# Optimization experiments

Hardware: AMD Instinct MI355X
Metric: run time of the kernel (lower is better)

Reference implementation:

```python
import jax, jax.numpy as jnp
import numpy as np

C = 128  # hidden_dim


def setup_inputs() -> dict:
    key = jax.random.key(0)
    ks = jax.random.split(key, 8)
    B, H, W = 4, 64, 64
    x1 = jax.random.normal(ks[0], (B, C, H, W), dtype=jnp.float32)
    x2 = jax.random.normal(ks[1], (B, C, H, W), dtype=jnp.float32)
    # 1x1 conv == per-pixel linear over channels; store weights as [C_out, C_in]
    s = 1.0 / np.sqrt(C)
    wq = jax.random.uniform(ks[2], (C, C), jnp.float32, -s, s)
    bq = jax.random.uniform(ks[3], (C,), jnp.float32, -s, s)
    wk = jax.random.uniform(ks[4], (C, C), jnp.float32, -s, s)
    bk = jax.random.uniform(ks[5], (C,), jnp.float32, -s, s)
    wv = jax.random.uniform(ks[6], (C, C), jnp.float32, -s, s)
    bv = jax.random.uniform(ks[7], (C,), jnp.float32, -s, s)
    return {"x1": x1, "x2": x2, "wq": wq, "bq": bq, "wk": wk, "bk": bk, "wv": wv, "bv": bv}


def reference(x1, x2, wq, bq, wk, bk, wv, bv):
    B, Cc, H, W = x1.shape
    N = H * W
    # flatten spatial -> tokens: [B, N, C]
    t1 = x1.reshape(B, Cc, N).transpose(0, 2, 1)
    t2 = x2.reshape(B, Cc, N).transpose(0, 2, 1)
    # 1x1 conv projections (per-token linear)
    q = jnp.einsum('bnc,oc->bno', t1, wq) + bq
    k = jnp.einsum('bnc,oc->bno', t2, wk) + bk
    v = jnp.einsum('bnc,oc->bno', t2, wv) + bv
    scale = 1.0 / jnp.sqrt(jnp.asarray(Cc, x1.dtype))
    attn = jax.nn.softmax(jnp.einsum('bqc,bkc->bqk', q, k) * scale, axis=-1)
    out = jnp.einsum('bqk,bkc->bqc', attn, v)  # [B, N, C]
    out = out.transpose(0, 2, 1).reshape(B, Cc, H, W)
    return out + x1
```

## Files before the change

### kernel.cpp

```cpp
#include <hip/hip_runtime.h>
#include <hip/hip_bf16.h>

typedef float  f32x4  __attribute__((ext_vector_type(4)));
typedef float  f32x16 __attribute__((ext_vector_type(16)));
typedef short  s16x8  __attribute__((ext_vector_type(8)));
typedef int    i32x8  __attribute__((ext_vector_type(8)));
typedef unsigned int   u32x2 __attribute__((ext_vector_type(2)));
typedef unsigned int   u32x4 __attribute__((ext_vector_type(4)));

#define B_ 4
#define C_ 128
#define N_ 4096
#define NST 16
#define QSCALE 0.12751744f

__device__ __forceinline__ unsigned int pkbf(float lo, float hi) {
    union { float f; unsigned int u; } a, b; a.f = lo; b.f = hi;
    return __builtin_amdgcn_perm(b.u + 0x8000u, a.u + 0x8000u, 0x07060302u);
}
__device__ __forceinline__ unsigned int pk_fp8x4(float a, float b, float c, float d) {
    int v = __builtin_amdgcn_cvt_pk_fp8_f32(a, b, 0, false);
    v = __builtin_amdgcn_cvt_pk_fp8_f32(c, d, v, true);
    return (unsigned int)v;
}
__device__ __forceinline__ unsigned int enc_fp4(float v) {
    float m = __builtin_fabsf(v);
    unsigned int c = 0;
    c += m > 0.25f; c += m > 0.75f; c += m > 1.25f; c += m > 1.75f;
    c += m > 2.5f;  c += m > 3.5f;  c += m > 5.0f;
    return c | ((__float_as_uint(v) >> 28) & 8u);
}
__device__ __forceinline__ unsigned int fp4x4(float a, float b, float c, float d) {
    return enc_fp4(a) | (enc_fp4(b) << 4) | (enc_fp4(c) << 8) | (enc_fp4(d) << 12);
}
__device__ __forceinline__ s16x8 mk_frag(unsigned int a, unsigned int b,
                                         unsigned int c, unsigned int d) {
    union { u32x4 u; s16x8 v; } t; t.u = (u32x4){a, b, c, d}; return t.v;
}
__device__ __forceinline__ f32x16 z16() {
    f32x16 v;
    #pragma unroll
    for (int r = 0; r < 16; r++) v[r] = 0.f;
    return v;
}
__device__ __forceinline__ i32x8 ld32g(const unsigned char* p) {
    union { u32x4 q[2]; i32x8 v; } t;
    t.q[0] = *(const u32x4*)p;
    t.q[1] = *(const u32x4*)(p + 1024);
    return t.v;
}
__device__ __forceinline__ i32x8 ld16g(const unsigned char* p) {
    union { u32x4 q[2]; i32x8 v; } t;
    t.q[0] = *(const u32x4*)p;
    t.q[1] = (u32x4){0u, 0u, 0u, 0u};
    return t.v;
}
__device__ __forceinline__ f32x16 mfs4(i32x8 a, i32x8 b, f32x16 c) {
    return __builtin_amdgcn_mfma_scale_f32_32x32x64_f8f6f4(
        a, b, c, 4, 0, 0, 0x7F7F7F7Fu, 0, 0x7F7F7F7Fu);
}

__global__ __launch_bounds__(256) void wcvt_kernel(
    const float* __restrict__ wq, const float* __restrict__ wk,
    const float* __restrict__ wv, unsigned short* __restrict__ Wf)
{
    const int gid = blockIdx.x * 256 + threadIdx.x;
    const int l = gid & 63, fid = gid >> 6;
    const int kc = fid & 7, ot = (fid >> 3) & 3, z = fid >> 5;
    const float* w = (z == 0) ? wq : (z == 1 ? wk : wv);
    const int o  = 32 * ot + (l & 31);
    const int c0 = 16 * kc + 8 * (l >> 5);
    const float* src = &w[o * C_ + c0];
    *(u32x4*)&Wf[fid * 512 + l * 8] = (u32x4){
        pkbf(src[0], src[1]), pkbf(src[2], src[3]),
        pkbf(src[4], src[5]), pkbf(src[6], src[7])};
}

__global__ __launch_bounds__(256, 2) void proj_kernel(
    const float* __restrict__ x1, const float* __restrict__ x2,
    const float* __restrict__ bq, const float* __restrict__ bk,
    const float* __restrict__ bv,
    const unsigned short* __restrict__ Wf,
    unsigned char* __restrict__ Qf, unsigned char* __restrict__ Kf,
    unsigned char* __restrict__ Vf)
{
    __shared__ float Xs[2][C_ * 36];
    const int tid = threadIdx.x;
    const int ot  = tid >> 6;
    const int l = tid & 63, lo = l & 31, h = l >> 5;
    const int bid = blockIdx.x;
    const int b = bid & 3, tb = bid >> 2;
    const int n0 = tb * 32;

    {
        const int q = tid & 7, c0 = tid >> 3;
        #pragma unroll
        for (int cc = 0; cc < 4; cc++) {
            const int c = c0 + 32 * cc;
            const size_t gof = ((size_t)b * C_ + c) * N_ + n0 + 4 * q;
            *(f32x4*)&Xs[0][c * 36 + 4 * q] = *(const f32x4*)&x1[gof];
            *(f32x4*)&Xs[1][c * 36 + 4 * q] = *(const f32x4*)&x2[gof];
        }
    }
    __syncthreads();

    auto ldW = [&](int z, int kc) -> s16x8 {
        return *(const s16x8*)&Wf[(((z * 4 + ot) * 8) + kc) * 512 + l * 8];
    };
    auto xfrag = [&](int z, int kc) -> s16x8 {
        const float* p = &Xs[z][(16 * kc + 8 * h) * 36 + lo];
        float f[8];
        #pragma unroll
        for (int i = 0; i < 8; i++) f[i] = p[i * 36];
        return mk_frag(pkbf(f[0], f[1]), pkbf(f[2], f[3]),
                       pkbf(f[4], f[5]), pkbf(f[6], f[7]));
    };

    f32x16 aq = z16(), ak = z16(), av = z16();
    s16x8 wqA = ldW(0, 0), wkA = ldW(1, 0), wvA = ldW(2, 0);
    s16x8 wqB, wkB, wvB;
    #pragma unroll
    for (int kc = 0; kc < 8; kc++) {
        if (kc & 1) {
            if (kc < 7) { wqA = ldW(0, kc + 1); wkA = ldW(1, kc + 1); wvA = ldW(2, kc + 1); }
            s16x8 f1 = xfrag(0, kc), f2 = xfrag(1, kc);
            aq = __builtin_amdgcn_mfma_f32_32x32x16_bf16(wqB, f1, aq, 0, 0, 0);
            ak = __builtin_amdgcn_mfma_f32_32x32x16_bf16(wkB, f2, ak, 0, 0, 0);
            av = __builtin_amdgcn_mfma_f32_32x32x16_bf16(f2, wvB, av, 0, 0, 0);
        } else {
            if (kc < 7) { wqB = ldW(0, kc + 1); wkB = ldW(1, kc + 1); wvB = ldW(2, kc + 1); }
            s16x8 f1 = xfrag(0, kc), f2 = xfrag(1, kc);
            aq = __builtin_amdgcn_mfma_f32_32x32x16_bf16(wqA, f1, aq, 0, 0, 0);
            ak = __builtin_amdgcn_mfma_f32_32x32x16_bf16(wkA, f2, ak, 0, 0, 0);
            av = __builtin_amdgcn_mfma_f32_32x32x16_bf16(f2, wvA, av, 0, 0, 0);
        }
    }

    const size_t fbase = (size_t)(b * 128 + tb) * 4096;
    #pragma unroll
    for (int rq = 0; rq < 4; rq++) {
        const int o0 = 32 * ot + 8 * rq + 4 * h;
        const f32x4 b4q = *(const f32x4*)&bq[o0];
        const size_t off = fbase + (ot >> 1) * 2048 + (rq >> 1) * 1024
                         + ((ot & 1) * 32 + lo) * 16 + 8 * (rq & 1) + 4 * h;
        *(unsigned int*)&Qf[off] = pk_fp8x4(
            (aq[4*rq+0] + b4q[0]) * QSCALE, (aq[4*rq+1] + b4q[1]) * QSCALE,
            (aq[4*rq+2] + b4q[2]) * QSCALE, (aq[4*rq+3] + b4q[3]) * QSCALE);
    }
    {
        const size_t kbase4 = (size_t)(b * 128 + tb) * 2048 + (size_t)(ot >> 1) * 1024
                            + (size_t)((ot & 1) * 32 + lo) * 16 + 2 * h;
        #pragma unroll
        for (int rq = 0; rq < 4; rq++) {
            const int o0 = 32 * ot + 8 * rq + 4 * h;
            const f32x4 b4k = *(const f32x4*)&bk[o0];
            *(unsigned short*)&Kf[kbase4 + 4 * rq] = (unsigned short)fp4x4(
                ak[4*rq+0] + b4k[0], ak[4*rq+1] + b4k[1],
                ak[4*rq+2] + b4k[2], ak[4*rq+3] + b4k[3]);
        }
    }
    {
        const float bvv = bv[32 * ot + lo];
        const size_t vbase4 = ((size_t)(b * 64 + (tb >> 1)) * 4 + ot) * 1024
                            + (size_t)((tb & 1) * 32 + lo) * 16 + 2 * h;
        #pragma unroll
        for (int rq = 0; rq < 4; rq++)
            *(unsigned short*)&Vf[vbase4 + 4 * rq] = (unsigned short)fp4x4(
                av[4*rq+0] + bvv, av[4*rq+1] + bvv,
                av[4*rq+2] + bvv, av[4*rq+3] + bvv);
    }
}

__global__ __launch_bounds__(512, 2) void attn_kernel(
    const unsigned char* __restrict__ Qf,
    const unsigned char* __restrict__ Kf,
    const unsigned char* __restrict__ Vf,
    const float* __restrict__ x1,
    float* __restrict__ out)
{
    __shared__ float Ol[4 * 128 * 33];
    __shared__ float Llds[8][32];

    const int tid = threadIdx.x;
    const int w  = tid >> 6;
    const int qi = w & 1, ps = w >> 1;
    const int l = tid & 63, lo = l & 31, h = l >> 5;
    const int bid = blockIdx.x;
    const int xcd = bid & 7, slot = bid >> 3;
    const int b  = xcd >> 1;
    const int qt = ((xcd & 1) << 5) | slot;
    const int q0 = qt * 64;

    const unsigned char* Kb = Kf + (size_t)b * 262144 + 2 * ps * 2048 + l * 16;
    const unsigned char* Vb = Vf + (size_t)b * 262144 + ps * 4096 + l * 16;

    i32x8 qb0, qb1;
    {
        const unsigned char* qp = Qf + (size_t)(b * 128 + qt * 2 + qi) * 4096 + l * 16;
        qb0 = ld32g(qp);
        qb1 = ld32g(qp + 2048);
    }

    f32x16 oacc[4];
    #pragma unroll
    for (int ct = 0; ct < 4; ct++) oacc[ct] = z16();
    float La = 0.f, Lb2 = 0.f;

    auto softmax_pack = [&](const f32x16& s0, const f32x16& s1) -> i32x8 {
        float e0[16], e1[16];
        #pragma unroll
        for (int r = 0; r < 16; r++) {
            e0[r] = __builtin_amdgcn_exp2f(s0[r]);
            e1[r] = __builtin_amdgcn_exp2f(s1[r]);
        }
        #pragma unroll
        for (int r = 0; r < 8; r++) { La += e0[r] + e1[r]; Lb2 += e0[r+8] + e1[r+8]; }
        union { unsigned int u[8]; i32x8 v; } pb;
        #pragma unroll
        for (int j = 0; j < 4; j++) {
            const unsigned int w0 = pk_fp8x4(e0[4*j], e0[4*j+1], e0[4*j+2], e0[4*j+3]);
            const unsigned int w1 = pk_fp8x4(e1[4*j], e1[4*j+1], e1[4*j+2], e1[4*j+3]);
            u32x2 sw = __builtin_amdgcn_permlane32_swap(w0, w1, false, false);
            pb.u[2*j]   = sw[0];
            pb.u[2*j+1] = sw[1];
        }
        return pb.v;
    };

    i32x8 k0, k1, k2, k3, v0, v1, v2, v3, pB;

    {
        const unsigned char* Kg = Kb + (size_t)(slot & 15) * 16384;
        k0 = ld16g(Kg);        k1 = ld16g(Kg + 1024);
        k2 = ld16g(Kg + 2048); k3 = ld16g(Kg + 3072);
        f32x16 s0 = z16(), s1 = z16();
        s0 = mfs4(k0, qb0, s0);
        s0 = mfs4(k1, qb1, s0);
        s1 = mfs4(k2, qb0, s1);
        s1 = mfs4(k3, qb1, s1);
        const unsigned char* Vg = Vb + (size_t)(slot & 15) * 16384;
        v0 = ld16g(Vg);        v1 = ld16g(Vg + 1024);
        v2 = ld16g(Vg + 2048); v3 = ld16g(Vg + 3072);
        const unsigned char* Kn = Kb + (size_t)((1 + slot) & 15) * 16384;
        k0 = ld16g(Kn);        k1 = ld16g(Kn + 1024);
        k2 = ld16g(Kn + 2048); k3 = ld16g(Kn + 3072);
        pB = softmax_pack(s0, s1);
    }

    #pragma unroll 2
    for (int t = 1; t < NST; t++) {
        f32x16 s0 = z16(), s1 = z16();
        oacc[0] = mfs4(v0, pB, oacc[0]);
        s0 = mfs4(k0, qb0, s0);
        oacc[1] = mfs4(v1, pB, oacc[1]);
        s0 = mfs4(k1, qb1, s0);
        oacc[2] = mfs4(v2, pB, oacc[2]);
        s1 = mfs4(k2, qb0, s1);
        oacc[3] = mfs4(v3, pB, oacc[3]);
        s1 = mfs4(k3, qb1, s1);
        const unsigned char* Vg = Vb + (size_t)((t + slot) & 15) * 16384;
        v0 = ld16g(Vg);        v1 = ld16g(Vg + 1024);
        v2 = ld16g(Vg + 2048); v3 = ld16g(Vg + 3072);
        if (t + 1 < NST) {
            const unsigned char* Kn = Kb + (size_t)((t + 1 + slot) & 15) * 16384;
            k0 = ld16g(Kn);        k1 = ld16g(Kn + 1024);
            k2 = ld16g(Kn + 2048); k3 = ld16g(Kn + 3072);
        }
        pB = softmax_pack(s0, s1);
    }
    oacc[0] = mfs4(v0, pB, oacc[0]);
    oacc[1] = mfs4(v1, pB, oacc[1]);
    oacc[2] = mfs4(v2, pB, oacc[2]);
    oacc[3] = mfs4(v3, pB, oacc[3]);

    const float Lh = La + Lb2;
    const float Lsum = Lh + __shfl_xor(Lh, 32, 64);
    if (l < 32) Llds[w][lo] = Lsum;
    __syncthreads();

    for (int g = 0; g < 2; g++) {
        if (qi == g) {
            #pragma unroll
            for (int ct = 0; ct < 4; ct++)
                #pragma unroll
                for (int r = 0; r < 16; r++) {
                    const int c = 32 * ct + (r & 3) + 8 * (r >> 2) + 4 * h;
                    Ol[ps * 4224 + c * 33 + lo] = oacc[ct][r];
                }
        }
        __syncthreads();
        {
            const int c = tid >> 2, qq = tid & 3;
            const size_t gbase = ((size_t)b * C_ + c) * N_ + q0 + g * 32 + qq * 8;
            float v[8];
            #pragma unroll
            for (int j = 0; j < 8; j++) {
                const int q = qq * 8 + j;
                const float ssum = Ol[c * 33 + q]        + Ol[4224  + c * 33 + q]
                                 + Ol[8448 + c * 33 + q] + Ol[12672 + c * 33 + q];
                const float Lq = Llds[g][q] + Llds[2 + g][q]
                               + Llds[4 + g][q] + Llds[6 + g][q];
                v[j] = ssum * __builtin_amdgcn_rcpf(Lq);
            }
            const f32x4 xlo = *(const f32x4*)&x1[gbase];
            const f32x4 xhi = *(const f32x4*)&x1[gbase + 4];
            *(f32x4*)&out[gbase]     = (f32x4){v[0]+xlo[0], v[1]+xlo[1], v[2]+xlo[2], v[3]+xlo[3]};
            *(f32x4*)&out[gbase + 4] = (f32x4){v[4]+xhi[0], v[5]+xhi[1], v[6]+xhi[2], v[7]+xhi[3]};
        }
        __syncthreads();
    }
}

extern "C" void kernel_launch(void* const* d_in, const int* in_sizes, int n_in,
                              void* d_out, int out_size, void* d_ws, size_t ws_size,
                              hipStream_t stream)
{
    const float* x1 = (const float*)d_in[0];
    const float* x2 = (const float*)d_in[1];
    const float* wq = (const float*)d_in[2];
    const float* bq = (const float*)d_in[3];
    const float* wk = (const float*)d_in[4];
    const float* bk = (const float*)d_in[5];
    const float* wv = (const float*)d_in[6];
    const float* bv = (const float*)d_in[7];
    float* out = (float*)d_out;

    unsigned short* Wf = (unsigned short*)d_ws;
    unsigned char* Qf = (unsigned char*)d_ws + 98304;
    unsigned char* Kf = Qf + (size_t)B_ * 128 * 4096;
    unsigned char* Vf = Kf + (size_t)B_ * 128 * 2048;

    wcvt_kernel<<<24, 256, 0, stream>>>(wq, wk, wv, Wf);
    proj_kernel<<<512, 256, 0, stream>>>(x1, x2, bq, bk, bv, Wf, Qf, Kf, Vf);
    attn_kernel<<<256, 512, 0, stream>>>(Qf, Kf, Vf, x1, out);
}
```

Measured before the change: 37.28 us.

## Fuse weight conversion into projection and single-pass attention epilogue

Drops the separate weight-conversion kernel: the projection kernel now reads fp32 weights directly and packs them to bf16 in registers. The X tile in LDS is stored token-major so fragments come from two vector LDS reads instead of eight strided scalar reads. The attention epilogue doubles its LDS output buffer so both query halves are written at once, which cuts two sync rounds down to one. The cost is redundant weight conversion in every projection block, transposed scalar LDS stores, and more LDS per attention block, which may lower occupancy.

```diff
diff --git a/kernel.cpp b/kernel.cpp
--- a/kernel.cpp
+++ b/kernel.cpp
@@ -60,31 +60,15 @@
         a, b, c, 4, 0, 0, 0x7F7F7F7Fu, 0, 0x7F7F7F7Fu);
 }
 
-__global__ __launch_bounds__(256) void wcvt_kernel(
-    const float* __restrict__ wq, const float* __restrict__ wk,
-    const float* __restrict__ wv, unsigned short* __restrict__ Wf)
-{
-    const int gid = blockIdx.x * 256 + threadIdx.x;
-    const int l = gid & 63, fid = gid >> 6;
-    const int kc = fid & 7, ot = (fid >> 3) & 3, z = fid >> 5;
-    const float* w = (z == 0) ? wq : (z == 1 ? wk : wv);
-    const int o  = 32 * ot + (l & 31);
-    const int c0 = 16 * kc + 8 * (l >> 5);
-    const float* src = &w[o * C_ + c0];
-    *(u32x4*)&Wf[fid * 512 + l * 8] = (u32x4){
-        pkbf(src[0], src[1]), pkbf(src[2], src[3]),
-        pkbf(src[4], src[5]), pkbf(src[6], src[7])};
-}
-
 __global__ __launch_bounds__(256, 2) void proj_kernel(
     const float* __restrict__ x1, const float* __restrict__ x2,
-    const float* __restrict__ bq, const float* __restrict__ bk,
-    const float* __restrict__ bv,
-    const unsigned short* __restrict__ Wf,
+    const float* __restrict__ wq, const float* __restrict__ bq,
+    const float* __restrict__ wk, const float* __restrict__ bk,
+    const float* __restrict__ wv, const float* __restrict__ bv,
     unsigned char* __restrict__ Qf, unsigned char* __restrict__ Kf,
     unsigned char* __restrict__ Vf)
 {
-    __shared__ float Xs[2][C_ * 36];
+    __shared__ float Xs[2][32][132];
     const int tid = threadIdx.x;
     const int ot  = tid >> 6;
     const int l = tid & 63, lo = l & 31, h = l >> 5;
@@ -98,42 +82,43 @@
         for (int cc = 0; cc < 4; cc++) {
             const int c = c0 + 32 * cc;
             const size_t gof = ((size_t)b * C_ + c) * N_ + n0 + 4 * q;
-            *(f32x4*)&Xs[0][c * 36 + 4 * q] = *(const f32x4*)&x1[gof];
-            *(f32x4*)&Xs[1][c * 36 + 4 * q] = *(const f32x4*)&x2[gof];
+            const f32x4 v1 = *(const f32x4*)&x1[gof];
+            const f32x4 v2 = *(const f32x4*)&x2[gof];
+            #pragma unroll
+            for (int j = 0; j < 4; j++) {
+                Xs[0][4 * q + j][c] = v1[j];
+                Xs[1][4 * q + j][c] = v2[j];
+            }
         }
     }
     __syncthreads();
 
-    auto ldW = [&](int z, int kc) -> s16x8 {
-        return *(const s16x8*)&Wf[(((z * 4 + ot) * 8) + kc) * 512 + l * 8];
+    auto wfrag = [&](const float* __restrict__ wp, int kc) -> s16x8 {
+        const float* p = &wp[(32 * ot + lo) * C_ + 16 * kc + 8 * h];
+        const f32x4 a = *(const f32x4*)p;
+        const f32x4 b2 = *(const f32x4*)(p + 4);
+        return mk_frag(pkbf(a[0], a[1]), pkbf(a[2], a[3]),
+                       pkbf(b2[0], b2[1]), pkbf(b2[2], b2[3]));
     };
     auto xfrag = [&](int z, int kc) -> s16x8 {
-        const float* p = &Xs[z][(16 * kc + 8 * h) * 36 + lo];
-        float f[8];
-        #pragma unroll
-        for (int i = 0; i < 8; i++) f[i] = p[i * 36];
-        return mk_frag(pkbf(f[0], f[1]), pkbf(f[2], f[3]),
-                       pkbf(f[4], f[5]), pkbf(f[6], f[7]));
+        const float* p = &Xs[z][lo][16 * kc + 8 * h];
+        const f32x4 a = *(const f32x4*)p;
+        const f32x4 b2 = *(const f32x4*)(p + 4);
+        return mk_frag(pkbf(a[0], a[1]), pkbf(a[2], a[3]),
+                       pkbf(b2[0], b2[1]), pkbf(b2[2], b2[3]));
     };
 
     f32x16 aq = z16(), ak = z16(), av = z16();
-    s16x8 wqA = ldW(0, 0), wkA = ldW(1, 0), wvA = ldW(2, 0);
-    s16x8 wqB, wkB, wvB;
     #pragma unroll
     for (int kc = 0; kc < 8; kc++) {
-        if (kc & 1) {
-            if (kc < 7) { wqA = ldW(0, kc + 1); wkA = ldW(1, kc + 1); wvA = ldW(2, kc + 1); }
-            s16x8 f1 = xfrag(0, kc), f2 = xfrag(1, kc);
-            aq = __builtin_amdgcn_mfma_f32_32x32x16_bf16(wqB, f1, aq, 0, 0, 0);
-            ak = __builtin_amdgcn_mfma_f32_32x32x16_bf16(wkB, f2, ak, 0, 0, 0);
-            av = __builtin_amdgcn_mfma_f32_32x32x16_bf16(f2, wvB, av, 0, 0, 0);
-        } else {
-            if (kc < 7) { wqB = ldW(0, kc + 1); wkB = ldW(1, kc + 1); wvB = ldW(2, kc + 1); }
-            s16x8 f1 = xfrag(0, kc), f2 = xfrag(1, kc);
-            aq = __builtin_amdgcn_mfma_f32_32x32x16_bf16(wqA, f1, aq, 0, 0, 0);
-            ak = __builtin_amdgcn_mfma_f32_32x32x16_bf16(wkA, f2, ak, 0, 0, 0);
-            av = __builtin_amdgcn_mfma_f32_32x32x16_bf16(f2, wvA, av, 0, 0, 0);
-        }
+        const s16x8 fwq = wfrag(wq, kc);
+        const s16x8 fwk = wfrag(wk, kc);
+        const s16x8 fwv = wfrag(wv, kc);
+        const s16x8 f1 = xfrag(0, kc);
+        const s16x8 f2 = xfrag(1, kc);
+        aq = __builtin_amdgcn_mfma_f32_32x32x16_bf16(fwq, f1, aq, 0, 0, 0);
+        ak = __builtin_amdgcn_mfma_f32_32x32x16_bf16(fwk, f2, ak, 0, 0, 0);
+        av = __builtin_amdgcn_mfma_f32_32x32x16_bf16(f2, fwv, av, 0, 0, 0);
     }
 
     const size_t fbase = (size_t)(b * 128 + tb) * 4096;
@@ -178,7 +163,7 @@
     const float* __restrict__ x1,
     float* __restrict__ out)
 {
-    __shared__ float Ol[4 * 128 * 33];
+    __shared__ float Ol8[8 * 128 * 33];
     __shared__ float Llds[8][32];
 
     const int tid = threadIdx.x;
@@ -276,38 +261,39 @@
     const float Lh = La + Lb2;
     const float Lsum = Lh + __shfl_xor(Lh, 32, 64);
     if (l < 32) Llds[w][lo] = Lsum;
+    {
+        float* slice = &Ol8[(qi * 4 + ps) * 4224];
+        #pragma unroll
+        for (int ct = 0; ct < 4; ct++)
+            #pragma unroll
+            for (int r = 0; r < 16; r++) {
+                const int c = 32 * ct + (r & 3) + 8 * (r >> 2) + 4 * h;
+                slice[c * 33 + lo] = oacc[ct][r];
+            }
+    }
     __syncthreads();
-
-    for (int g = 0; g < 2; g++) {
-        if (qi == g) {
-            #pragma unroll
-            for (int ct = 0; ct < 4; ct++)
-                #pragma unroll
-                for (int r = 0; r < 16; r++) {
-                    const int c = 32 * ct + (r & 3) + 8 * (r >> 2) + 4 * h;
-                    Ol[ps * 4224 + c * 33 + lo] = oacc[ct][r];
-                }
-        }
-        __syncthreads();
-        {
-            const int c = tid >> 2, qq = tid & 3;
-            const size_t gbase = ((size_t)b * C_ + c) * N_ + q0 + g * 32 + qq * 8;
-            float v[8];
-            #pragma unroll
-            for (int j = 0; j < 8; j++) {
-                const int q = qq * 8 + j;
-                const float ssum = Ol[c * 33 + q]        + Ol[4224  + c * 33 + q]
-                                 + Ol[8448 + c * 33 + q] + Ol[12672 + c * 33 + q];
-                const float Lq = Llds[g][q] + Llds[2 + g][q]
-                               + Llds[4 + g][q] + Llds[6 + g][q];
-                v[j] = ssum * __builtin_amdgcn_rcpf(Lq);
-            }
-            const f32x4 xlo = *(const f32x4*)&x1[gbase];
-            const f32x4 xhi = *(const f32x4*)&x1[gbase + 4];
-            *(f32x4*)&out[gbase]     = (f32x4){v[0]+xlo[0], v[1]+xlo[1], v[2]+xlo[2], v[3]+xlo[3]};
-            *(f32x4*)&out[gbase + 4] = (f32x4){v[4]+xhi[0], v[5]+xhi[1], v[6]+xhi[2], v[7]+xhi[3]};
-        }
-        __syncthreads();
+    {
+        const int g   = tid >> 8;
+        const int rem = tid & 255;
+        const int c   = rem >> 1;
+        const int qh  = rem & 1;
+        const float* base = &Ol8[g * 4 * 4224 + c * 33 + 16 * qh];
+        float vv[16];
+        #pragma unroll
+        for (int j = 0; j < 16; j++) {
+            const int q = 16 * qh + j;
+            const float ssum = base[j] + base[4224 + j] + base[8448 + j] + base[12672 + j];
+            const float Lq = Llds[g][q] + Llds[2 + g][q] + Llds[4 + g][q] + Llds[6 + g][q];
+            vv[j] = ssum * __builtin_amdgcn_rcpf(Lq);
+        }
+        const size_t gbase = ((size_t)b * C_ + c) * N_ + q0 + 32 * g + 16 * qh;
+        #pragma unroll
+        for (int s4 = 0; s4 < 4; s4++) {
+            const f32x4 xr = *(const f32x4*)&x1[gbase + 4 * s4];
+            *(f32x4*)&out[gbase + 4 * s4] = (f32x4){
+                vv[4*s4+0] + xr[0], vv[4*s4+1] + xr[1],
+                vv[4*s4+2] + xr[2], vv[4*s4+3] + xr[3]};
+        }
     }
 }
 
@@ -325,12 +311,10 @@
     const float* bv = (const float*)d_in[7];
     float* out = (float*)d_out;
 
-    unsigned short* Wf = (unsigned short*)d_ws;
-    unsigned char* Qf = (unsigned char*)d_ws + 98304;
+    unsigned char* Qf = (unsigned char*)d_ws;
     unsigned char* Kf = Qf + (size_t)B_ * 128 * 4096;
     unsigned char* Vf = Kf + (size_t)B_ * 128 * 2048;
 
-    wcvt_kernel<<<24, 256, 0, stream>>>(wq, wk, wv, Wf);
-    proj_kernel<<<512, 256, 0, stream>>>(x1, x2, bq, bk, bv, Wf, Qf, Kf, Vf);
+    proj_kernel<<<512, 256, 0, stream>>>(x1, x2, wq, bq, wk, bk, wv, bv, Qf, Kf, Vf);
     attn_kernel<<<256, 512, 0, stream>>>(Qf, Kf, Vf, x1, out);
 }
```

After: 41.76 us. 1.12x slower.
